# Optimization experiments

Hardware: AMD Instinct MI355X
Metric: run time of the kernel (lower is better)

Reference implementation:

```python
import jax, jax.numpy as jnp
import numpy as np

HEADS = 8
DIM_HEAD = 64
INNER = HEADS * DIM_HEAD  # 512
EPS = 1e-6


def layer_norm(x, gamma, beta):
    mu = jnp.mean(x, axis=-1, keepdims=True)
    var = jnp.var(x, axis=-1, keepdims=True)
    return (x - mu) * jax.lax.rsqrt(var + EPS) * gamma + beta


def setup_inputs() -> dict:
    key = jax.random.key(0)
    ks = jax.random.split(key, 8)
    b, n = 2, 2048
    s = lambda d: 1.0 / np.sqrt(d)
    return {
        "x": jax.random.normal(ks[0], (b, n, INNER), dtype=jnp.float32),
        # weights stored input-major: y = x @ W
        "w_qkv": jax.random.normal(ks[1], (INNER, 3 * INNER), dtype=jnp.float32) * s(INNER),
        "w_out": jax.random.normal(ks[2], (INNER, INNER), dtype=jnp.float32) * s(INNER),
        "b_out": jax.random.normal(ks[3], (INNER,), dtype=jnp.float32) * 0.01,
        "w_ff1": jax.random.normal(ks[4], (INNER, 4 * INNER), dtype=jnp.float32) * s(INNER),
        "w_ff2": jax.random.normal(ks[5], (4 * INNER, INNER), dtype=jnp.float32) * s(4 * INNER),
        "g1": jnp.ones((INNER,), dtype=jnp.float32),
        "be1": jnp.zeros((INNER,), dtype=jnp.float32),
        "g2": jnp.ones((INNER,), dtype=jnp.float32),
        "be2": jnp.zeros((INNER,), dtype=jnp.float32),
    }


def reference(x, w_qkv, w_out, b_out, w_ff1, w_ff2, g1, be1, g2, be2):
    b, n, _ = x.shape
    scale = DIM_HEAD ** (-0.5)
    qkv = x @ w_qkv  # [b, n, 3*inner]
    qkv = qkv.reshape(b, n, 3, HEADS, DIM_HEAD)
    q = qkv[:, :, 0].transpose(0, 2, 1, 3)  # [b, h, n, d]
    k = qkv[:, :, 1].transpose(0, 2, 1, 3)
    v = qkv[:, :, 2].transpose(0, 2, 1, 3)
    dots = jnp.einsum('bhqd,bhkd->bhqk', q, k) * scale
    attn = jax.nn.softmax(dots, axis=-1)
    out = jnp.einsum('bhqk,bhkd->bhqd', attn, v)
    out = out.transpose(0, 2, 1, 3).reshape(b, n, INNER)
    out = out @ w_out + b_out
    attn_res = layer_norm(x + out, g1, be1)
    # NOTE: no activation between the two FFN linears (faithful to source)
    ff = (attn_res @ w_ff1) @ w_ff2
    return layer_norm(attn_res + ff, g2, be2)
```

## Files before the change

kernel.cpp:

```cpp
#include <hip/hip_runtime.h>
#include <hip/hip_bf16.h>
#include <cstdint>
#include <cstddef>
#include <math.h>

#define HEADS 8
#define DHEAD 64
#define INNER 512
#define BATCH 2
#define SEQ   2048
#define MROWS (BATCH*SEQ)
#define LN_EPS 1e-6f
#define KSPLIT 4
#define KCHUNK (SEQ/KSPLIT)

typedef unsigned short u16;
typedef __attribute__((ext_vector_type(8))) short short8;
typedef __attribute__((ext_vector_type(4))) short short4v;
typedef __attribute__((ext_vector_type(4))) float f32x4;

#define MFMA16(a,b,c) __builtin_amdgcn_mfma_f32_16x16x32_bf16((a),(b),(c),0,0,0)
#if __has_builtin(__builtin_amdgcn_mfma_f32_16x16x16bf16_1k)
#define HAVE_MFMA16K16 1
#define MFMA16K16(a,b,c) __builtin_amdgcn_mfma_f32_16x16x16bf16_1k((a),(b),(c),0,0,0)
#endif

__device__ __forceinline__ float bf2f(u16 u) {
    union { float f; uint32_t i; } x; x.i = ((uint32_t)u) << 16; return x.f;
}
__device__ __forceinline__ u16 f2bf(float f) {
    __hip_bfloat16 h = __float2bfloat16(f);
    return *reinterpret_cast<u16*>(&h);
}
__device__ __forceinline__ void gl_lds16(const void* g, void* l) {
    __builtin_amdgcn_global_load_lds(
        (const __attribute__((address_space(1))) void*)g,
        (__attribute__((address_space(3))) void*)l, 16, 0, 0);
}

__global__ void prep_kernel(const float* __restrict__ x, u16* __restrict__ x_b,
                            const float* __restrict__ w_qkv, u16* __restrict__ w_qkvT,
                            const float* __restrict__ w_out, u16* __restrict__ w_outT,
                            const float* __restrict__ w_ff1, u16* __restrict__ w_ff1T,
                            const float* __restrict__ w_ff2, u16* __restrict__ w_ff2T) {
    __shared__ float T[32][33];
    const int blk = blockIdx.x, tid = threadIdx.x;
    if (blk < 2048) {
        int i = blk * 256 + tid;
        float4 v = reinterpret_cast<const float4*>(x)[i];
        ushort4 o;
        o.x = f2bf(v.x); o.y = f2bf(v.y); o.z = f2bf(v.z); o.w = f2bf(v.w);
        reinterpret_cast<ushort4*>(x_b)[i] = o;
        return;
    }
    const float* B; u16* Bt; int K, N, t;
    if (blk < 2816)      { B = w_qkv; Bt = w_qkvT; K = 512;  N = 1536; t = blk - 2048; }
    else if (blk < 3072) { B = w_out; Bt = w_outT; K = 512;  N = 512;  t = blk - 2816; }
    else if (blk < 4096) { B = w_ff1; Bt = w_ff1T; K = 512;  N = 2048; t = blk - 3072; }
    else                 { B = w_ff2; Bt = w_ff2T; K = 2048; N = 512;  t = blk - 4096; }
    const int nb = N / 32;
    const int n0 = (t % nb) * 32, k0 = (t / nb) * 32;
    const int r = tid >> 3, c = (tid & 7) * 4;
    float4 v = *reinterpret_cast<const float4*>(&B[(size_t)(k0 + r) * N + n0 + c]);
    T[c + 0][r] = v.x; T[c + 1][r] = v.y; T[c + 2][r] = v.z; T[c + 3][r] = v.w;
    __syncthreads();
    ushort4 o;
    o.x = f2bf(T[r][c + 0]); o.y = f2bf(T[r][c + 1]);
    o.z = f2bf(T[r][c + 2]); o.w = f2bf(T[r][c + 3]);
    *reinterpret_cast<ushort4*>(&Bt[(size_t)(n0 + r) * K + k0 + c]) = o;
}

template<int BN, int EPI>
__global__ __launch_bounds__(256) void gemm_bt(const u16* __restrict__ A,
                                               const u16* __restrict__ Bt,
                                               const float* __restrict__ bias,
                                               float* __restrict__ C,
                                               u16* __restrict__ Cb,
                                               u16* __restrict__ Vt,
                                               int M, int N, int K) {
    constexpr int WN = BN / 2;
    constexpr int NT = WN / 16;
    __shared__ u16 As[128 * 32];
    __shared__ u16 Bs[BN * 32];
    const int tid = threadIdx.x;
    const int wave = tid >> 6, lane = tid & 63;
    const int l15 = lane & 15, quad = lane >> 4;
    const int wm = (wave >> 1) * 64, wn = (wave & 1) * WN;
    const int row0 = blockIdx.y * 128, col0 = blockIdx.x * BN;

    int kbase = 0, kend = K;
    if (EPI == 3) {
        int chunk = K / gridDim.z;
        kbase = blockIdx.z * chunk; kend = kbase + chunk;
    }

    f32x4 acc[4][NT];
    #pragma unroll
    for (int mi = 0; mi < 4; ++mi)
        #pragma unroll
        for (int ni = 0; ni < NT; ++ni)
            #pragma unroll
            for (int e = 0; e < 4; ++e) acc[mi][ni][e] = 0.f;

    for (int k0 = kbase; k0 < kend; k0 += 32) {
        #pragma unroll
        for (int idx0 = 0; idx0 < 512 + BN * 4; idx0 += 256) {
            int idx = idx0 + tid;
            if (idx < 512) {
                int r = idx >> 2, ic = (idx & 3) * 8;
                gl_lds16(A + (size_t)(row0 + r) * K + k0 + ic, &As[idx * 8]);
            } else {
                int ib = idx - 512;
                int r = ib >> 2, ic = (ib & 3) * 8;
                gl_lds16(Bt + (size_t)(col0 + r) * K + k0 + ic, &Bs[ib * 8]);
            }
        }
        __syncthreads();

        short8 af[4], bf[NT];
        #pragma unroll
        for (int mi = 0; mi < 4; ++mi)
            af[mi] = *reinterpret_cast<const short8*>(&As[(wm + mi * 16 + l15) * 32 + quad * 8]);
        #pragma unroll
        for (int ni = 0; ni < NT; ++ni)
            bf[ni] = *reinterpret_cast<const short8*>(&Bs[(wn + ni * 16 + l15) * 32 + quad * 8]);
        #pragma unroll
        for (int mi = 0; mi < 4; ++mi)
            #pragma unroll
            for (int ni = 0; ni < NT; ++ni)
                acc[mi][ni] = MFMA16(af[mi], bf[ni], acc[mi][ni]);
        __syncthreads();
    }

    #pragma unroll
    for (int mi = 0; mi < 4; ++mi)
        #pragma unroll
        for (int ni = 0; ni < NT; ++ni) {
            const int cc = col0 + wn + ni * 16 + l15;
            const int rr0 = row0 + wm + mi * 16 + quad * 4;
            if (EPI == 0) {
                #pragma unroll
                for (int r = 0; r < 4; ++r)
                    Cb[(size_t)(rr0 + r) * N + cc] = f2bf(acc[mi][ni][r]);
            } else if (EPI == 1) {
                #pragma unroll
                for (int r = 0; r < 4; ++r)
                    C[(size_t)(rr0 + r) * N + cc] = acc[mi][ni][r] + bias[cc];
            } else if (EPI == 3) {
                float* Cz = C + (size_t)blockIdx.z * M * N;
                #pragma unroll
                for (int r = 0; r < 4; ++r)
                    Cz[(size_t)(rr0 + r) * N + cc] = acc[mi][ni][r];
            } else {
                if (cc < 1024) {
                    size_t base = (cc < 512) ? (size_t)cc
                                             : ((size_t)MROWS * 512 + cc - 512);
                    #pragma unroll
                    for (int r = 0; r < 4; ++r)
                        Cb[base + (size_t)(rr0 + r) * 512] = f2bf(acc[mi][ni][r]);
                } else {
                    int hh = (cc - 1024) >> 6, dd = (cc - 1024) & 63;
                    int bb = rr0 >> 11, srow = rr0 & 2047;
                    ushort4 o;
                    o.x = f2bf(acc[mi][ni][0]); o.y = f2bf(acc[mi][ni][1]);
                    o.z = f2bf(acc[mi][ni][2]); o.w = f2bf(acc[mi][ni][3]);
                    *reinterpret_cast<ushort4*>(
                        &Vt[(((size_t)(bb * 8 + hh) * 64 + dd) << 11) + srow]) = o;
                }
            }
        }
}

__global__ __launch_bounds__(256) void attn_kernel(const u16* __restrict__ qk_b,
                                                   const u16* __restrict__ vT_b,
                                                   u16* __restrict__ OpartB,
                                                   float* __restrict__ lpart) {
    __shared__ u16 SM[3 * 64 * 72];
    u16 (*Qs)[72] = (u16(*)[72])SM;
    u16 (*Ks)[72] = (u16(*)[72])(SM + 64 * 72);
    u16 (*VT)[72] = (u16(*)[72])(SM + 2 * 64 * 72);

    const int tid = threadIdx.x;
    const int wave = tid >> 6, lane = tid & 63;
    const int l15 = lane & 15, quad = lane >> 4;
    const int qt = blockIdx.x, bh = blockIdx.y, ks = blockIdx.z;
    const int b = bh >> 3, h = bh & 7;
    const int w16 = wave * 16;
    const int r0 = tid >> 3, r1 = r0 + 32;
    const int ch = (tid & 7) * 8;

    {
        const u16* qb = qk_b + (size_t)(b * SEQ + qt * 64) * 512 + h * 64;
        *reinterpret_cast<uint4*>(&Qs[r0][ch]) =
            *reinterpret_cast<const uint4*>(&qb[(size_t)r0 * 512 + ch]);
        *reinterpret_cast<uint4*>(&Qs[r1][ch]) =
            *reinterpret_cast<const uint4*>(&qb[(size_t)r1 * 512 + ch]);
    }
    __syncthreads();

    short8 qf[2];
    qf[0] = *reinterpret_cast<const short8*>(&Qs[w16 + l15][quad * 8]);
    qf[1] = *reinterpret_cast<const short8*>(&Qs[w16 + l15][32 + quad * 8]);

    const u16* kb = qk_b + (size_t)MROWS * 512
                  + (size_t)(b * SEQ + ks * KCHUNK) * 512 + h * 64;
    const u16* vb = vT_b + (size_t)bh * 64 * 2048 + ks * KCHUNK;

    uint4 kr0 = *reinterpret_cast<const uint4*>(&kb[(size_t)r0 * 512 + ch]);
    uint4 kr1 = *reinterpret_cast<const uint4*>(&kb[(size_t)r1 * 512 + ch]);
    uint4 vr0 = *reinterpret_cast<const uint4*>(&vb[(size_t)r0 * 2048 + ch]);
    uint4 vr1 = *reinterpret_cast<const uint4*>(&vb[(size_t)r1 * 2048 + ch]);

    const float CEXP = 0.18033688011110918f;

#ifdef HAVE_MFMA16K16
    f32x4 oacc[4];
    float lsum = 0.f;
    #pragma unroll
    for (int di = 0; di < 4; ++di)
        #pragma unroll
        for (int e = 0; e < 4; ++e) oacc[di][e] = 0.f;

    for (int kt = 0; kt < KCHUNK / 64; ++kt) {
        *reinterpret_cast<uint4*>(&Ks[r0][ch]) = kr0;
        *reinterpret_cast<uint4*>(&Ks[r1][ch]) = kr1;
        *reinterpret_cast<uint4*>(&VT[r0][ch]) = vr0;
        *reinterpret_cast<uint4*>(&VT[r1][ch]) = vr1;
        __syncthreads();

        if (kt + 1 < KCHUNK / 64) {
            const u16* kb2 = kb + (size_t)(kt + 1) * 64 * 512;
            const u16* vb2 = vb + (kt + 1) * 64;
            kr0 = *reinterpret_cast<const uint4*>(&kb2[(size_t)r0 * 512 + ch]);
            kr1 = *reinterpret_cast<const uint4*>(&kb2[(size_t)r1 * 512 + ch]);
            vr0 = *reinterpret_cast<const uint4*>(&vb2[(size_t)r0 * 2048 + ch]);
            vr1 = *reinterpret_cast<const uint4*>(&vb2[(size_t)r1 * 2048 + ch]);
        }

        f32x4 sacc[4];
        #pragma unroll
        for (int ni = 0; ni < 4; ++ni)
            #pragma unroll
            for (int e = 0; e < 4; ++e) sacc[ni][e] = 0.f;
        #pragma unroll
        for (int ksk = 0; ksk < 2; ++ksk) {
            short8 kf[4];
            #pragma unroll
            for (int ni = 0; ni < 4; ++ni)
                kf[ni] = *reinterpret_cast<const short8*>(
                    &Ks[ni * 16 + l15][ksk * 32 + quad * 8]);
            #pragma unroll
            for (int ni = 0; ni < 4; ++ni)
                sacc[ni] = MFMA16(kf[ni], qf[ksk], sacc[ni]);
        }

        #pragma unroll
        for (int ni = 0; ni < 4; ++ni) {
            short4v pp;
            #pragma unroll
            for (int r = 0; r < 4; ++r) {
                float p = exp2f(sacc[ni][r] * CEXP);
                lsum += p;
                pp[r] = (short)f2bf(p);
            }
            #pragma unroll
            for (int di = 0; di < 4; ++di) {
                short4v vf = *reinterpret_cast<const short4v*>(
                    &VT[di * 16 + l15][ni * 16 + quad * 4]);
                oacc[di] = MFMA16K16(vf, pp, oacc[di]);
            }
        }
        __syncthreads();
    }

    lsum += __shfl_xor(lsum, 16);
    lsum += __shfl_xor(lsum, 32);

    const size_t pbase = ((size_t)(ks * 16 + bh) * SEQ + qt * 64);
    if (lane < 16) lpart[pbase + w16 + lane] = lsum;

    float* OTf = (float*)SM;
    #pragma unroll
    for (int di = 0; di < 4; ++di)
        #pragma unroll
        for (int r = 0; r < 4; ++r)
            OTf[(di * 16 + quad * 4 + r) * 68 + w16 + l15] = oacc[di][r];
    __syncthreads();

    const int ql = tid >> 2, dseg = (tid & 3) * 16;
    u16 ov[16];
    #pragma unroll
    for (int i = 0; i < 16; ++i) ov[i] = f2bf(OTf[(dseg + i) * 68 + ql]);
    u16* op = &OpartB[(pbase + ql) * 64 + dseg];
    *reinterpret_cast<uint4*>(op)     = *reinterpret_cast<const uint4*>(ov);
    *reinterpret_cast<uint4*>(op + 8) = *reinterpret_cast<const uint4*>(ov + 8);
#else
    f32x4 oacc[4];
    float lsum[4];
    #pragma unroll
    for (int di = 0; di < 4; ++di)
        #pragma unroll
        for (int e = 0; e < 4; ++e) oacc[di][e] = 0.f;
    #pragma unroll
    for (int r = 0; r < 4; ++r) lsum[r] = 0.f;

    for (int kt = 0; kt < KCHUNK / 64; ++kt) {
        *reinterpret_cast<uint4*>(&Ks[r0][ch]) = kr0;
        *reinterpret_cast<uint4*>(&Ks[r1][ch]) = kr1;
        *reinterpret_cast<uint4*>(&VT[r0][ch]) = vr0;
        *reinterpret_cast<uint4*>(&VT[r1][ch]) = vr1;
        __syncthreads();

        if (kt + 1 < KCHUNK / 64) {
            const u16* kb2 = kb + (size_t)(kt + 1) * 64 * 512;
            const u16* vb2 = vb + (kt + 1) * 64;
            kr0 = *reinterpret_cast<const uint4*>(&kb2[(size_t)r0 * 512 + ch]);
            kr1 = *reinterpret_cast<const uint4*>(&kb2[(size_t)r1 * 512 + ch]);
            vr0 = *reinterpret_cast<const uint4*>(&vb2[(size_t)r0 * 2048 + ch]);
            vr1 = *reinterpret_cast<const uint4*>(&vb2[(size_t)r1 * 2048 + ch]);
        }

        f32x4 sacc[4];
        #pragma unroll
        for (int ni = 0; ni < 4; ++ni)
            #pragma unroll
            for (int e = 0; e < 4; ++e) sacc[ni][e] = 0.f;
        #pragma unroll
        for (int ksk = 0; ksk < 2; ++ksk) {
            short8 kf[4];
            #pragma unroll
            for (int ni = 0; ni < 4; ++ni)
                kf[ni] = *reinterpret_cast<const short8*>(
                    &Ks[ni * 16 + l15][ksk * 32 + quad * 8]);
            #pragma unroll
            for (int ni = 0; ni < 4; ++ni)
                sacc[ni] = MFMA16(qf[ksk], kf[ni], sacc[ni]);
        }
        #pragma unroll
        for (int ni = 0; ni < 4; ++ni)
            #pragma unroll
            for (int r = 0; r < 4; ++r) {
                float p = exp2f(sacc[ni][r] * CEXP);
                lsum[r] += p;
                Qs[w16 + quad * 4 + r][ni * 16 + l15] = f2bf(p);
            }
        #pragma unroll
        for (int ksk = 0; ksk < 2; ++ksk) {
            short8 pf = *reinterpret_cast<const short8*>(
                &Qs[w16 + l15][ksk * 32 + quad * 8]);
            #pragma unroll
            for (int di = 0; di < 4; ++di) {
                short8 vf = *reinterpret_cast<const short8*>(
                    &VT[di * 16 + l15][ksk * 32 + quad * 8]);
                oacc[di] = MFMA16(pf, vf, oacc[di]);
            }
        }
        __syncthreads();
    }

    #pragma unroll
    for (int r = 0; r < 4; ++r) {
        float v = lsum[r];
        v += __shfl_xor(v, 1); v += __shfl_xor(v, 2);
        v += __shfl_xor(v, 4); v += __shfl_xor(v, 8);
        lsum[r] = v;
    }
    const size_t pbase = ((size_t)(ks * 16 + bh) * SEQ + qt * 64);
    #pragma unroll
    for (int di = 0; di < 4; ++di)
        #pragma unroll
        for (int r = 0; r < 4; ++r)
            OpartB[(pbase + w16 + quad * 4 + r) * 64 + di * 16 + l15] = f2bf(oacc[di][r]);
    if (l15 == 0)
        #pragma unroll
        for (int r = 0; r < 4; ++r)
            lpart[pbase + w16 + quad * 4 + r] = lsum[r];
#endif
}

__global__ void attn_combine_kernel(const u16* __restrict__ OpartB,
                                    const float* __restrict__ lpart,
                                    u16* __restrict__ attn_b) {
    int i = blockIdx.x * 256 + threadIdx.x;
    int e = i * 4;
    int row = e >> 9;
    int c = e & 511;
    int h = c >> 6, d = c & 63;
    int b = row >> 11, srow = row & 2047;
    int bh = b * 8 + h;

    float ax = 0.f, ay = 0.f, az = 0.f, aw = 0.f, l = 0.f;
    #pragma unroll
    for (int ks = 0; ks < KSPLIT; ++ks) {
        size_t pk = (size_t)(ks * 16 + bh) * SEQ + srow;
        ushort4 o = *reinterpret_cast<const ushort4*>(&OpartB[pk * 64 + d]);
        ax += bf2f(o.x); ay += bf2f(o.y); az += bf2f(o.z); aw += bf2f(o.w);
        l += lpart[pk];
    }
    float li = 1.f / l;
    ushort4 o;
    o.x = f2bf(ax * li); o.y = f2bf(ay * li);
    o.z = f2bf(az * li); o.w = f2bf(aw * li);
    *reinterpret_cast<ushort4*>(&attn_b[(size_t)row * INNER + c]) = o;
}

template<bool A16, bool TWO>
__global__ void ln_kernel(const void* __restrict__ a_,
                          const float* __restrict__ s0,
                          const float* __restrict__ s1,
                          const float* __restrict__ g,
                          const float* __restrict__ be,
                          float* __restrict__ out32,
                          u16* __restrict__ out16) {
    __shared__ float red[256];
    const int row = blockIdx.x, tid = threadIdx.x;
    const size_t off = (size_t)row * INNER;
    const int c0 = tid, c1 = tid + 256;

    float a0, a1;
    if (A16) {
        const u16* a = (const u16*)a_;
        a0 = bf2f(a[off + c0]); a1 = bf2f(a[off + c1]);
    } else {
        const float* a = (const float*)a_;
        a0 = a[off + c0]; a1 = a[off + c1];
    }
    float v0 = a0 + s0[off + c0];
    float v1 = a1 + s0[off + c1];
    if (TWO) { v0 += s1[off + c0]; v1 += s1[off + c1]; }

    red[tid] = v0 + v1;
    __syncthreads();
    for (int s = 128; s > 0; s >>= 1) {
        if (tid < s) red[tid] += red[tid + s];
        __syncthreads();
    }
    float mu = red[0] * (1.f / INNER);
    __syncthreads();

    float d0 = v0 - mu, d1 = v1 - mu;
    red[tid] = d0 * d0 + d1 * d1;
    __syncthreads();
    for (int s = 128; s > 0; s >>= 1) {
        if (tid < s) red[tid] += red[tid + s];
        __syncthreads();
    }
    float rstd = rsqrtf(red[0] * (1.f / INNER) + LN_EPS);

    float y0 = d0 * rstd * g[c0] + be[c0];
    float y1 = d1 * rstd * g[c1] + be[c1];
    if (out32) { out32[off + c0] = y0; out32[off + c1] = y1; }
    if (out16) { out16[off + c0] = f2bf(y0); out16[off + c1] = f2bf(y1); }
}

extern "C" void kernel_launch(void* const* d_in, const int* in_sizes, int n_in,
                              void* d_out, int out_size, void* d_ws, size_t ws_size,
                              hipStream_t stream) {
    const float* x     = (const float*)d_in[0];
    const float* w_qkv = (const float*)d_in[1];
    const float* w_out = (const float*)d_in[2];
    const float* b_out = (const float*)d_in[3];
    const float* w_ff1 = (const float*)d_in[4];
    const float* w_ff2 = (const float*)d_in[5];
    const float* g1    = (const float*)d_in[6];
    const float* be1   = (const float*)d_in[7];
    const float* g2    = (const float*)d_in[8];
    const float* be2   = (const float*)d_in[9];
    float* out = (float*)d_out;

    char* W = (char*)d_ws;
    u16*   w_outT     = (u16*)  (W + 0);
    u16*   w_ff1T     = (u16*)  (W + 524288);
    u16*   w_ff2T     = (u16*)  (W + 2621440);
    u16*   qk_b       = (u16*)  (W + 4718592);
    u16*   attn_b     = (u16*)  (W + 4718592);
    u16*   attn_res_b = (u16*)  (W + 4718592);
    float* proj       = (float*)(W + 8912896);
    u16*   ff1_b      = (u16*)  (W + 8912896);
    u16*   vT_b       = (u16*)  (W + 13107200);
    u16*   x_b        = (u16*)  (W + 17301504);
    u16*   w_qkvT     = (u16*)  (W + 21495808);
    u16*   OpartB     = (u16*)  (W + 17301504);
    float* lpart      = (float*)(W + 34078720);
    float* ff2p       = (float*)(W + 25690112);

    prep_kernel<<<5120, 256, 0, stream>>>(x, x_b, w_qkv, w_qkvT, w_out, w_outT,
                                          w_ff1, w_ff1T, w_ff2, w_ff2T);

    gemm_bt<128, 2><<<dim3(1536 / 128, MROWS / 128), 256, 0, stream>>>(
        x_b, w_qkvT, nullptr, nullptr, qk_b, vT_b, MROWS, 1536, INNER);

    attn_kernel<<<dim3(SEQ / 64, BATCH * HEADS, KSPLIT), 256, 0, stream>>>(
        qk_b, vT_b, OpartB, lpart);

    attn_combine_kernel<<<(MROWS * INNER / 4) / 256, 256, 0, stream>>>(
        OpartB, lpart, attn_b);

    gemm_bt<64, 1><<<dim3(INNER / 64, MROWS / 128), 256, 0, stream>>>(
        attn_b, w_outT, b_out, proj, nullptr, nullptr, MROWS, INNER, INNER);

    ln_kernel<false, false><<<MROWS, 256, 0, stream>>>(
        x, proj, nullptr, g1, be1, nullptr, attn_res_b);

    gemm_bt<128, 0><<<dim3(2048 / 128, MROWS / 128), 256, 0, stream>>>(
        attn_res_b, w_ff1T, nullptr, nullptr, ff1_b, nullptr, MROWS, 2048, INNER);

    gemm_bt<64, 3><<<dim3(INNER / 64, MROWS / 128, 2), 256, 0, stream>>>(
        ff1_b, w_ff2T, nullptr, ff2p, nullptr, nullptr, MROWS, INNER, 2048);

    ln_kernel<true, true><<<MROWS, 256, 0, stream>>>(
        attn_res_b, ff2p, ff2p + (size_t)MROWS * INNER, g2, be2, out, nullptr);
}
```

Before: 223.6 us.

## Fuse attention combine into projection GEMM, wave-per-row layernorm, bf16 split-K partials

Removes the separate attention-combine kernel by reducing the split-K attention partials while loading the A operand of a new 64x64 projection GEMM. LayerNorm is rewritten to handle one row per wave using shuffle reductions and vectorised loads, replacing the block-wide shared-memory tree. The FF2 split-K partials are now stored in bf16 to halve that traffic, the QKV GEMM uses narrower tiles to launch more blocks, and the attention Q tile drops its padding. Workspace buffers are re-aliased to match. The risks are extra precision loss in the bf16 partials and redundant combine work, since each projection block re-reads the partials for its own columns.

After: 233.1 us. +4.3%, slower.

```diff
diff --git a/kernel.cpp b/kernel.cpp
--- a/kernel.cpp
+++ b/kernel.cpp
@@ -73,8 +73,6 @@
 template<int BN, int EPI>
 __global__ __launch_bounds__(256) void gemm_bt(const u16* __restrict__ A,
                                                const u16* __restrict__ Bt,
-                                               const float* __restrict__ bias,
-                                               float* __restrict__ C,
                                                u16* __restrict__ Cb,
                                                u16* __restrict__ Vt,
                                                int M, int N, int K) {
@@ -117,18 +115,18 @@
         }
         __syncthreads();
 
-        short8 af[4], bf[NT];
+        short8 af[4], bfr[NT];
         #pragma unroll
         for (int mi = 0; mi < 4; ++mi)
             af[mi] = *reinterpret_cast<const short8*>(&As[(wm + mi * 16 + l15) * 32 + quad * 8]);
         #pragma unroll
         for (int ni = 0; ni < NT; ++ni)
-            bf[ni] = *reinterpret_cast<const short8*>(&Bs[(wn + ni * 16 + l15) * 32 + quad * 8]);
+            bfr[ni] = *reinterpret_cast<const short8*>(&Bs[(wn + ni * 16 + l15) * 32 + quad * 8]);
         #pragma unroll
         for (int mi = 0; mi < 4; ++mi)
             #pragma unroll
             for (int ni = 0; ni < NT; ++ni)
-                acc[mi][ni] = MFMA16(af[mi], bf[ni], acc[mi][ni]);
+                acc[mi][ni] = MFMA16(af[mi], bfr[ni], acc[mi][ni]);
         __syncthreads();
     }
 
@@ -142,15 +140,11 @@
                 #pragma unroll
                 for (int r = 0; r < 4; ++r)
                     Cb[(size_t)(rr0 + r) * N + cc] = f2bf(acc[mi][ni][r]);
-            } else if (EPI == 1) {
+            } else if (EPI == 3) {
+                u16* Cz = Cb + (size_t)blockIdx.z * M * N;
                 #pragma unroll
                 for (int r = 0; r < 4; ++r)
-                    C[(size_t)(rr0 + r) * N + cc] = acc[mi][ni][r] + bias[cc];
-            } else if (EPI == 3) {
-                float* Cz = C + (size_t)blockIdx.z * M * N;
-                #pragma unroll
-                for (int r = 0; r < 4; ++r)
-                    Cz[(size_t)(rr0 + r) * N + cc] = acc[mi][ni][r];
+                    Cz[(size_t)(rr0 + r) * N + cc] = f2bf(acc[mi][ni][r]);
             } else {
                 if (cc < 1024) {
                     size_t base = (cc < 512) ? (size_t)cc
@@ -171,14 +165,91 @@
         }
 }
 
+__global__ __launch_bounds__(256) void gemm_proj(const u16* __restrict__ OpartB,
+                                                 const float* __restrict__ lpart,
+                                                 const u16* __restrict__ Bt,
+                                                 const float* __restrict__ bias,
+                                                 float* __restrict__ C) {
+    __shared__ u16 As[64 * 32];
+    __shared__ u16 Bs[64 * 32];
+    const int tid = threadIdx.x;
+    const int wave = tid >> 6, lane = tid & 63;
+    const int l15 = lane & 15, quad = lane >> 4;
+    const int wm = (wave >> 1) * 32, wn = (wave & 1) * 32;
+    const int row0 = blockIdx.y * 64, col0 = blockIdx.x * 64;
+
+    f32x4 acc[2][2];
+    #pragma unroll
+    for (int mi = 0; mi < 2; ++mi)
+        #pragma unroll
+        for (int ni = 0; ni < 2; ++ni)
+            #pragma unroll
+            for (int e = 0; e < 4; ++e) acc[mi][ni][e] = 0.f;
+
+    const int r = tid >> 2, ic = (tid & 3) * 8;
+    const int gr = row0 + r;
+    const int bb = gr >> 11, srow = gr & 2047;
+
+    for (int k0 = 0; k0 < 512; k0 += 32) {
+        gl_lds16(Bt + (size_t)(col0 + r) * 512 + k0 + ic, &Bs[tid * 8]);
+        {
+            const int gc = k0 + ic;
+            const int h = gc >> 6, d0 = gc & 63;
+            const int bh = bb * 8 + h;
+            float l = 0.f, o[8] = {0.f, 0.f, 0.f, 0.f, 0.f, 0.f, 0.f, 0.f};
+            #pragma unroll
+            for (int ks = 0; ks < KSPLIT; ++ks) {
+                size_t pk = ((size_t)(ks * 16 + bh) << 11) + srow;
+                l += lpart[pk];
+                uint4 uv = *reinterpret_cast<const uint4*>(&OpartB[pk * 64 + d0]);
+                const u16* up = (const u16*)&uv;
+                #pragma unroll
+                for (int i = 0; i < 8; ++i) o[i] += bf2f(up[i]);
+            }
+            float inv = 1.f / l;
+            u16 a8[8];
+            #pragma unroll
+            for (int i = 0; i < 8; ++i) a8[i] = f2bf(o[i] * inv);
+            *reinterpret_cast<uint4*>(&As[tid * 8]) =
+                *reinterpret_cast<const uint4*>(a8);
+        }
+        __syncthreads();
+
+        short8 af[2], bfr[2];
+        #pragma unroll
+        for (int mi = 0; mi < 2; ++mi)
+            af[mi] = *reinterpret_cast<const short8*>(&As[(wm + mi * 16 + l15) * 32 + quad * 8]);
+        #pragma unroll
+        for (int ni = 0; ni < 2; ++ni)
+            bfr[ni] = *reinterpret_cast<const short8*>(&Bs[(wn + ni * 16 + l15) * 32 + quad * 8]);
+        #pragma unroll
+        for (int mi = 0; mi < 2; ++mi)
+            #pragma unroll
+            for (int ni = 0; ni < 2; ++ni)
+                acc[mi][ni] = MFMA16(af[mi], bfr[ni], acc[mi][ni]);
+        __syncthreads();
+    }
+
+    #pragma unroll
+    for (int mi = 0; mi < 2; ++mi)
+        #pragma unroll
+        for (int ni = 0; ni < 2; ++ni) {
+            const int cc = col0 + wn + ni * 16 + l15;
+            const int rr0 = row0 + wm + mi * 16 + quad * 4;
+            #pragma unroll
+            for (int rr = 0; rr < 4; ++rr)
+                C[(size_t)(rr0 + rr) * 512 + cc] = acc[mi][ni][rr] + bias[cc];
+        }
+}
+
 __global__ __launch_bounds__(256) void attn_kernel(const u16* __restrict__ qk_b,
                                                    const u16* __restrict__ vT_b,
                                                    u16* __restrict__ OpartB,
                                                    float* __restrict__ lpart) {
-    __shared__ u16 SM[3 * 64 * 72];
-    u16 (*Qs)[72] = (u16(*)[72])SM;
-    u16 (*Ks)[72] = (u16(*)[72])(SM + 64 * 72);
-    u16 (*VT)[72] = (u16(*)[72])(SM + 2 * 64 * 72);
+    __shared__ u16 SM[64 * 64 + 2 * 64 * 72];
+    u16 (*Qs)[64] = (u16(*)[64])SM;
+    u16 (*Ks)[72] = (u16(*)[72])(SM + 64 * 64);
+    u16 (*VT)[72] = (u16(*)[72])(SM + 64 * 64 + 64 * 72);
 
     const int tid = threadIdx.x;
     const int wave = tid >> 6, lane = tid & 63;
@@ -378,79 +449,84 @@
 #endif
 }
 
-__global__ void attn_combine_kernel(const u16* __restrict__ OpartB,
-                                    const float* __restrict__ lpart,
-                                    u16* __restrict__ attn_b) {
-    int i = blockIdx.x * 256 + threadIdx.x;
-    int e = i * 4;
-    int row = e >> 9;
-    int c = e & 511;
-    int h = c >> 6, d = c & 63;
-    int b = row >> 11, srow = row & 2047;
-    int bh = b * 8 + h;
-
-    float ax = 0.f, ay = 0.f, az = 0.f, aw = 0.f, l = 0.f;
-    #pragma unroll
-    for (int ks = 0; ks < KSPLIT; ++ks) {
-        size_t pk = (size_t)(ks * 16 + bh) * SEQ + srow;
-        ushort4 o = *reinterpret_cast<const ushort4*>(&OpartB[pk * 64 + d]);
-        ax += bf2f(o.x); ay += bf2f(o.y); az += bf2f(o.z); aw += bf2f(o.w);
-        l += lpart[pk];
-    }
-    float li = 1.f / l;
-    ushort4 o;
-    o.x = f2bf(ax * li); o.y = f2bf(ay * li);
-    o.z = f2bf(az * li); o.w = f2bf(aw * li);
-    *reinterpret_cast<ushort4*>(&attn_b[(size_t)row * INNER + c]) = o;
-}
-
-template<bool A16, bool TWO>
-__global__ void ln_kernel(const void* __restrict__ a_,
-                          const float* __restrict__ s0,
-                          const float* __restrict__ s1,
-                          const float* __restrict__ g,
-                          const float* __restrict__ be,
-                          float* __restrict__ out32,
-                          u16* __restrict__ out16) {
-    __shared__ float red[256];
-    const int row = blockIdx.x, tid = threadIdx.x;
+template<bool A16, bool S16, bool TWO>
+__global__ __launch_bounds__(256) void ln_kernel(const void* __restrict__ a_,
+                                                 const void* __restrict__ s0_,
+                                                 const void* __restrict__ s1_,
+                                                 const float* __restrict__ g,
+                                                 const float* __restrict__ be,
+                                                 float* __restrict__ out32,
+                                                 u16* __restrict__ out16) {
+    const int tid = threadIdx.x, wave = tid >> 6, lane = tid & 63;
+    const int row = blockIdx.x * 4 + wave;
     const size_t off = (size_t)row * INNER;
-    const int c0 = tid, c1 = tid + 256;
-
-    float a0, a1;
-    if (A16) {
-        const u16* a = (const u16*)a_;
-        a0 = bf2f(a[off + c0]); a1 = bf2f(a[off + c1]);
-    } else {
-        const float* a = (const float*)a_;
-        a0 = a[off + c0]; a1 = a[off + c1];
-    }
-    float v0 = a0 + s0[off + c0];
-    float v1 = a1 + s0[off + c1];
-    if (TWO) { v0 += s1[off + c0]; v1 += s1[off + c1]; }
-
-    red[tid] = v0 + v1;
-    __syncthreads();
-    for (int s = 128; s > 0; s >>= 1) {
-        if (tid < s) red[tid] += red[tid + s];
-        __syncthreads();
-    }
-    float mu = red[0] * (1.f / INNER);
-    __syncthreads();
-
-    float d0 = v0 - mu, d1 = v1 - mu;
-    red[tid] = d0 * d0 + d1 * d1;
-    __syncthreads();
-    for (int s = 128; s > 0; s >>= 1) {
-        if (tid < s) red[tid] += red[tid + s];
-        __syncthreads();
-    }
-    float rstd = rsqrtf(red[0] * (1.f / INNER) + LN_EPS);
-
-    float y0 = d0 * rstd * g[c0] + be[c0];
-    float y1 = d1 * rstd * g[c1] + be[c1];
-    if (out32) { out32[off + c0] = y0; out32[off + c1] = y1; }
-    if (out16) { out16[off + c0] = f2bf(y0); out16[off + c1] = f2bf(y1); }
+
+    float v[8];
+    #pragma unroll
+    for (int j = 0; j < 2; ++j) {
+        const int c = j * 256 + lane * 4;
+        float a0, a1, a2, a3;
+        if (A16) {
+            ushort4 u = *reinterpret_cast<const ushort4*>((const u16*)a_ + off + c);
+            a0 = bf2f(u.x); a1 = bf2f(u.y); a2 = bf2f(u.z); a3 = bf2f(u.w);
+        } else {
+            float4 u = *reinterpret_cast<const float4*>((const float*)a_ + off + c);
+            a0 = u.x; a1 = u.y; a2 = u.z; a3 = u.w;
+        }
+        float s0, s1, s2, s3;
+        if (S16) {
+            ushort4 u = *reinterpret_cast<const ushort4*>((const u16*)s0_ + off + c);
+            s0 = bf2f(u.x); s1 = bf2f(u.y); s2 = bf2f(u.z); s3 = bf2f(u.w);
+        } else {
+            float4 u = *reinterpret_cast<const float4*>((const float*)s0_ + off + c);
+            s0 = u.x; s1 = u.y; s2 = u.z; s3 = u.w;
+        }
+        v[j*4+0] = a0 + s0; v[j*4+1] = a1 + s1; v[j*4+2] = a2 + s2; v[j*4+3] = a3 + s3;
+        if (TWO) {
+            if (S16) {
+                ushort4 u = *reinterpret_cast<const ushort4*>((const u16*)s1_ + off + c);
+                v[j*4+0] += bf2f(u.x); v[j*4+1] += bf2f(u.y);
+                v[j*4+2] += bf2f(u.z); v[j*4+3] += bf2f(u.w);
+            } else {
+                float4 u = *reinterpret_cast<const float4*>((const float*)s1_ + off + c);
+                v[j*4+0] += u.x; v[j*4+1] += u.y; v[j*4+2] += u.z; v[j*4+3] += u.w;
+            }
+        }
+    }
+
+    float s = 0.f;
+    #pragma unroll
+    for (int i = 0; i < 8; ++i) s += v[i];
+    #pragma unroll
+    for (int m = 1; m < 64; m <<= 1) s += __shfl_xor(s, m);
+    const float mu = s * (1.f / INNER);
+
+    float q = 0.f;
+    #pragma unroll
+    for (int i = 0; i < 8; ++i) { v[i] -= mu; q += v[i] * v[i]; }
+    #pragma unroll
+    for (int m = 1; m < 64; m <<= 1) q += __shfl_xor(q, m);
+    const float rstd = rsqrtf(q * (1.f / INNER) + LN_EPS);
+
+    #pragma unroll
+    for (int j = 0; j < 2; ++j) {
+        const int c = j * 256 + lane * 4;
+        float4 gv = *reinterpret_cast<const float4*>(g + c);
+        float4 bv = *reinterpret_cast<const float4*>(be + c);
+        float y0 = v[j*4+0] * rstd * gv.x + bv.x;
+        float y1 = v[j*4+1] * rstd * gv.y + bv.y;
+        float y2 = v[j*4+2] * rstd * gv.z + bv.z;
+        float y3 = v[j*4+3] * rstd * gv.w + bv.w;
+        if (out32) {
+            float4 o = {y0, y1, y2, y3};
+            *reinterpret_cast<float4*>(out32 + off + c) = o;
+        }
+        if (out16) {
+            ushort4 o;
+            o.x = f2bf(y0); o.y = f2bf(y1); o.z = f2bf(y2); o.w = f2bf(y3);
+            *reinterpret_cast<ushort4*>(out16 + off + c) = o;
+        }
+    }
 }
 
 extern "C" void kernel_launch(void* const* d_in, const int* in_sizes, int n_in,
@@ -473,41 +549,37 @@
     u16*   w_ff1T     = (u16*)  (W + 524288);
     u16*   w_ff2T     = (u16*)  (W + 2621440);
     u16*   qk_b       = (u16*)  (W + 4718592);
-    u16*   attn_b     = (u16*)  (W + 4718592);
-    u16*   attn_res_b = (u16*)  (W + 4718592);
-    float* proj       = (float*)(W + 8912896);
-    u16*   ff1_b      = (u16*)  (W + 8912896);
+    float* proj       = (float*)(W + 4718592);
+    u16*   ff2p       = (u16*)  (W + 4718592);
     u16*   vT_b       = (u16*)  (W + 13107200);
+    u16*   attn_res_b = (u16*)  (W + 13107200);
     u16*   x_b        = (u16*)  (W + 17301504);
     u16*   w_qkvT     = (u16*)  (W + 21495808);
     u16*   OpartB     = (u16*)  (W + 17301504);
+    u16*   ff1_b      = (u16*)  (W + 17301504);
     float* lpart      = (float*)(W + 34078720);
-    float* ff2p       = (float*)(W + 25690112);
 
     prep_kernel<<<5120, 256, 0, stream>>>(x, x_b, w_qkv, w_qkvT, w_out, w_outT,
                                           w_ff1, w_ff1T, w_ff2, w_ff2T);
 
-    gemm_bt<128, 2><<<dim3(1536 / 128, MROWS / 128), 256, 0, stream>>>(
-        x_b, w_qkvT, nullptr, nullptr, qk_b, vT_b, MROWS, 1536, INNER);
+    gemm_bt<64, 2><<<dim3(1536 / 64, MROWS / 128), 256, 0, stream>>>(
+        x_b, w_qkvT, qk_b, vT_b, MROWS, 1536, INNER);
 
     attn_kernel<<<dim3(SEQ / 64, BATCH * HEADS, KSPLIT), 256, 0, stream>>>(
         qk_b, vT_b, OpartB, lpart);
 
-    attn_combine_kernel<<<(MROWS * INNER / 4) / 256, 256, 0, stream>>>(
-        OpartB, lpart, attn_b);
-
-    gemm_bt<64, 1><<<dim3(INNER / 64, MROWS / 128), 256, 0, stream>>>(
-        attn_b, w_outT, b_out, proj, nullptr, nullptr, MROWS, INNER, INNER);
-
-    ln_kernel<false, false><<<MROWS, 256, 0, stream>>>(
+    gemm_proj<<<dim3(INNER / 64, MROWS / 64), 256, 0, stream>>>(
+        OpartB, lpart, w_outT, b_out, proj);
+
+    ln_kernel<false, false, false><<<MROWS / 4, 256, 0, stream>>>(
         x, proj, nullptr, g1, be1, nullptr, attn_res_b);
 
     gemm_bt<128, 0><<<dim3(2048 / 128, MROWS / 128), 256, 0, stream>>>(
-        attn_res_b, w_ff1T, nullptr, nullptr, ff1_b, nullptr, MROWS, 2048, INNER);
+        attn_res_b, w_ff1T, ff1_b, nullptr, MROWS, 2048, INNER);
 
     gemm_bt<64, 3><<<dim3(INNER / 64, MROWS / 128, 2), 256, 0, stream>>>(
-        ff1_b, w_ff2T, nullptr, ff2p, nullptr, nullptr, MROWS, INNER, 2048);
-
-    ln_kernel<true, true><<<MROWS, 256, 0, stream>>>(
+        ff1_b, w_ff2T, ff2p, nullptr, MROWS, INNER, 2048);
+
+    ln_kernel<true, true, true><<<MROWS / 4, 256, 0, stream>>>(
         attn_res_b, ff2p, ff2p + (size_t)MROWS * INNER, g2, be2, out, nullptr);
 }
```
